# Kernel optimization log

Measured on AMD Instinct MI355X. Metric: run time of the kernel, lower is better.

Reference implementation:

```python
import jax, jax.numpy as jnp
import numpy as np

B, N, K, D_MODEL = 4, 16384, 32, 64

def gather_neighbors(x, idx):
    # x: [B, N, F], idx: [B, N, K] -> [B, N, K, F]
    return jnp.take_along_axis(x[:, :, None, :], idx[:, :, :, None], axis=1)

def setup_inputs() -> dict:
    key = jax.random.key(0)
    k1, k2, k3, k4, k5 = jax.random.split(key, 5)
    x = jax.random.normal(k1, (B, N, D_MODEL), dtype=jnp.float32)
    pos = jax.random.normal(k2, (B, N, 3), dtype=jnp.float32)
    neighbor_idx = jax.random.randint(k3, (B, N, K), 0, N, dtype=jnp.int32)
    W1 = jax.random.normal(k4, (3, D_MODEL), dtype=jnp.float32) * (1.0 / np.sqrt(3.0))
    b1 = jnp.zeros((D_MODEL,), dtype=jnp.float32)
    W2 = jax.random.normal(k5, (D_MODEL, D_MODEL), dtype=jnp.float32) * (1.0 / np.sqrt(D_MODEL))
    b2 = jnp.zeros((D_MODEL,), dtype=jnp.float32)
    return {"x": x, "pos": pos, "neighbor_idx": neighbor_idx,
            "W1": W1, "b1": b1, "W2": W2, "b2": b2}

def reference(x, pos, neighbor_idx, W1, b1, W2, b2):
    # gather neighbor positions: [B, N, K, 3]
    neighbors = gather_neighbors(pos, neighbor_idx)
    rel_pos = pos[:, :, None, :] - neighbors              # [B, N, K, 3]
    # weight MLP: Linear(3,d) + LeakyReLU(0.1), Linear(d,d)
    h = jax.nn.leaky_relu(jnp.einsum('bnkd,df->bnkf', rel_pos, W1) + b1, 0.1)
    w = jnp.einsum('bnkf,fg->bnkg', h, W2) + b2           # [B, N, K, F]
    xg = gather_neighbors(x, neighbor_idx)                # [B, N, K, F]
    return jnp.sum(w * xg, axis=2)                        # [B, N, F]
```

## Files before the change

### kernel.cpp

```cpp
#include <hip/hip_runtime.h>


#define NPTS   16384
#define KNB    32
#define F      64
#define BATCH  4
#define LOG2N  14
#define WPTS   8

typedef _Float16 h2     __attribute__((ext_vector_type(2)));
typedef _Float16 h8     __attribute__((ext_vector_type(8)));
typedef float    f32x16 __attribute__((ext_vector_type(16)));

__global__ __launch_bounds__(256, 2) void pointconv_mfma(
    const float* __restrict__ x,
    const float* __restrict__ pos,
    const int*   __restrict__ idx,
    const float* __restrict__ W1,
    const float* __restrict__ b1,
    const float* __restrict__ W2,
    const float* __restrict__ b2,
    float*       __restrict__ out)
{
    __shared__ __align__(16) _Float16 w1p[32][8];
    __shared__ __align__(16) _Float16 w2f[2][4][2][32][8];

    const int tid = threadIdx.x;
    if (tid < 32) {
        const int g = 2 * tid;
        w1p[tid][0] = (_Float16)W1[0 * F + g]; w1p[tid][1] = (_Float16)W1[0 * F + g + 1];
        w1p[tid][2] = (_Float16)W1[1 * F + g]; w1p[tid][3] = (_Float16)W1[1 * F + g + 1];
        w1p[tid][4] = (_Float16)W1[2 * F + g]; w1p[tid][5] = (_Float16)W1[2 * F + g + 1];
        w1p[tid][6] = (_Float16)b1[g];         w1p[tid][7] = (_Float16)b1[g + 1];
    }
#pragma unroll
    for (int r = 0; r < 16; ++r) {
        const int e = r * 256 + tid;
        const int g = e >> 6, f = e & 63;
        w2f[(g >> 3) & 1][g >> 4][f & 1][f >> 1][g & 7] = (_Float16)W2[e];
    }
    __syncthreads();

    const int lane = tid & 63;
    const int wv   = tid >> 6;
    const int m    = lane & 31;
    const int hf   = lane >> 5;

    const float2 b2v = *(const float2*)(b2 + 2 * m);

    const int p0   = (blockIdx.x * 4 + wv) * WPTS;
    const int p0_s = __builtin_amdgcn_readfirstlane(p0);
    const int base = (p0_s >> LOG2N) << LOG2N;
    const float* __restrict__ xb2 = x + (size_t)base * F + 2 * m;

    int jlo[16], jhi[16];

    {
        const int* __restrict__ rowp = idx + (size_t)p0_s * KNB;
#pragma unroll
        for (int reg = 0; reg < 16; ++reg) {
            const int rA = (reg & 3) + ((reg >> 2) << 3);
            jlo[reg] = rowp[rA];
            jhi[reg] = rowp[rA + 4];
        }
    }
    float2 xvA[16], xvB[16];
#pragma unroll
    for (int reg = 0; reg < 16; ++reg) {
        const int jk = hf ? jhi[reg] : jlo[reg];
        xvA[reg] = *(const float2*)(xb2 + (size_t)jk * F);
    }

    float rx, ry, rz;
    {
        const int jm = idx[p0_s * KNB + m];
        const int nr = base + jm;
        rx = pos[p0_s * 3 + 0] - pos[nr * 3 + 0];
        ry = pos[p0_s * 3 + 1] - pos[nr * 3 + 1];
        rz = pos[p0_s * 3 + 2] - pos[nr * 3 + 2];
    }

    const h2 c01 = { (_Float16)0.1f, (_Float16)0.1f };

#define POINT_BODY(XV_CUR, XV_NXT, I)                                         \
    {                                                                         \
        const int p_s = p0_s + (I);                                           \
        const bool has_next = (I) + 1 < WPTS;                                 \
          \
        if (has_next) {                                                       \
            const int* __restrict__ rowp = idx + (size_t)(p_s + 1) * KNB;     \
            _Pragma("unroll")                                                 \
            for (int reg = 0; reg < 16; ++reg) {                              \
                const int rA = (reg & 3) + ((reg >> 2) << 3);                 \
                jlo[reg] = rowp[rA];                                          \
                jhi[reg] = rowp[rA + 4];                                      \
            }                                                                 \
        }                                                                     \
                                       \
        float rxn = 0.f, ryn = 0.f, rzn = 0.f;                                \
        if (has_next) {                                                       \
            const int jmn = idx[(p_s + 1) * KNB + m];                         \
            const int nr  = base + jmn;                                       \
            rxn = pos[(p_s + 1) * 3 + 0] - pos[nr * 3 + 0];                   \
            ryn = pos[(p_s + 1) * 3 + 1] - pos[nr * 3 + 1];                   \
            rzn = pos[(p_s + 1) * 3 + 2] - pos[nr * 3 + 2];                   \
        }                                                                     \
                      \
        f32x16 acc0, acc1;                                                    \
        _Pragma("unroll")                                                     \
        for (int r = 0; r < 16; ++r) { acc0[r] = b2v.x; acc1[r] = b2v.y; }    \
        const h2 rxp = { (_Float16)rx, (_Float16)rx };                        \
        const h2 ryp = { (_Float16)ry, (_Float16)ry };                        \
        const h2 rzp = { (_Float16)rz, (_Float16)rz };                        \
        _Pragma("unroll")                                                     \
        for (int t = 0; t < 4; ++t) {                                         \
            h8 af;                                                            \
            _Pragma("unroll")                                                 \
            for (int jj = 0; jj < 4; ++jj) {                                  \
                const int g2 = 8 * t + 4 * hf + jj;                           \
                const h8 w = *(const h8*)&w1p[g2][0];                         \
                const h2 wx = __builtin_shufflevector(w, w, 0, 1);            \
                const h2 wy = __builtin_shufflevector(w, w, 2, 3);            \
                const h2 wz = __builtin_shufflevector(w, w, 4, 5);            \
                const h2 bb = __builtin_shufflevector(w, w, 6, 7);            \
                h2 hv = bb + rxp * wx;                                        \
                hv = hv + ryp * wy;                                           \
                hv = hv + rzp * wz;                                           \
                hv = __builtin_elementwise_max(hv, hv * c01);                 \
                af[2 * jj]     = hv[0];                                       \
                af[2 * jj + 1] = hv[1];                                       \
            }                                                                 \
            const h8 bf0 = *(const h8*)&w2f[hf][t][0][m][0];                  \
            const h8 bf1 = *(const h8*)&w2f[hf][t][1][m][0];                  \
            acc0 = __builtin_amdgcn_mfma_f32_32x32x16_f16(af, bf0, acc0, 0, 0, 0); \
            acc1 = __builtin_amdgcn_mfma_f32_32x32x16_f16(af, bf1, acc1, 0, 0, 0); \
        }                                                                     \
              \
        if (has_next) {                                                       \
            _Pragma("unroll")                                                 \
            for (int reg = 0; reg < 16; ++reg) {                              \
                const int jk = hf ? jhi[reg] : jlo[reg];                      \
                XV_NXT[reg] = *(const float2*)(xb2 + (size_t)jk * F);         \
            }                                                                 \
        }                                                                     \
                 \
        float s0 = 0.f, s1 = 0.f;                                             \
        _Pragma("unroll")                                                     \
        for (int reg = 0; reg < 16; ++reg) {                                  \
            s0 = fmaf(acc0[reg], XV_CUR[reg].x, s0);                          \
            s1 = fmaf(acc1[reg], XV_CUR[reg].y, s1);                          \
        }                                                                     \
        s0 += __shfl_xor(s0, 32);                                             \
        s1 += __shfl_xor(s1, 32);                                             \
        if (hf == 0)                                                          \
            *(float2*)(out + (size_t)p_s * F + 2 * m) = make_float2(s0, s1);  \
        rx = rxn; ry = ryn; rz = rzn;                                         \
    }

#pragma unroll 1
    for (int io = 0; io < WPTS; io += 2) {
        POINT_BODY(xvA, xvB, io);
        POINT_BODY(xvB, xvA, io + 1);
    }
#undef POINT_BODY
}

extern "C" void kernel_launch(void* const* d_in, const int* in_sizes, int n_in,
                              void* d_out, int out_size, void* d_ws, size_t ws_size,
                              hipStream_t stream) {
    const float* x   = (const float*)d_in[0];
    const float* pos = (const float*)d_in[1];
    const int*   idx = (const int*)  d_in[2];
    const float* W1  = (const float*)d_in[3];
    const float* b1  = (const float*)d_in[4];
    const float* W2  = (const float*)d_in[5];
    const float* b2  = (const float*)d_in[6];
    float* out = (float*)d_out;

    dim3 grid((BATCH * NPTS) / (4 * WPTS));
    dim3 block(256);
    pointconv_mfma<<<grid, block, 0, stream>>>(x, pos, idx, W1, b1, W2, b2, out);
}
```

Measured before the change: 138.3 us.

## Broadcast neighbor indices via ds_bpermute and deepen index/pos prefetch pipeline

Measured after the change: 409.0 us. +195.6%, slower.

```diff
diff --git a/kernel.cpp b/kernel.cpp
--- a/kernel.cpp
+++ b/kernel.cpp
@@ -12,7 +12,7 @@
 typedef _Float16 h8     __attribute__((ext_vector_type(8)));
 typedef float    f32x16 __attribute__((ext_vector_type(16)));
 
-__global__ __launch_bounds__(256, 2) void pointconv_mfma(
+__global__ __launch_bounds__(256, 3) void pointconv_mfma(
     const float* __restrict__ x,
     const float* __restrict__ pos,
     const int*   __restrict__ idx,
@@ -45,6 +45,7 @@
     const int wv   = tid >> 6;
     const int m    = lane & 31;
     const int hf   = lane >> 5;
+    const int voff = hf << 4;
 
     const float2 b2v = *(const float2*)(b2 + 2 * m);
 
@@ -53,59 +54,53 @@
     const int base = (p0_s >> LOG2N) << LOG2N;
     const float* __restrict__ xb2 = x + (size_t)base * F + 2 * m;
 
-    int jlo[16], jhi[16];
+    const h2 c01 = { (_Float16)0.1f, (_Float16)0.1f };
 
+    float2 xvA[16], xvB[16];
+    float  rlA[6], rlB[6];
+    int    jmA = 0, jmB = 0;
     {
-        const int* __restrict__ rowp = idx + (size_t)p0_s * KNB;
+        const int jm0 = idx[p0_s * KNB + m];
 #pragma unroll
         for (int reg = 0; reg < 16; ++reg) {
             const int rA = (reg & 3) + ((reg >> 2) << 3);
-            jlo[reg] = rowp[rA];
-            jhi[reg] = rowp[rA + 4];
+            const int jk = __builtin_amdgcn_ds_bpermute(voff + 4 * rA, jm0);
+            xvA[reg] = *(const float2*)(xb2 + (size_t)jk * F);
         }
-    }
-    float2 xvA[16], xvB[16];
-#pragma unroll
-    for (int reg = 0; reg < 16; ++reg) {
-        const int jk = hf ? jhi[reg] : jlo[reg];
-        xvA[reg] = *(const float2*)(xb2 + (size_t)jk * F);
+        const int nr0 = base + jm0;
+        rlA[0] = pos[nr0 * 3 + 0]; rlA[1] = pos[nr0 * 3 + 1]; rlA[2] = pos[nr0 * 3 + 2];
+        rlA[3] = pos[p0_s * 3 + 0]; rlA[4] = pos[p0_s * 3 + 1]; rlA[5] = pos[p0_s * 3 + 2];
+        if (WPTS > 1) jmA = idx[(p0_s + 1) * KNB + m];
     }
 
-    float rx, ry, rz;
-    {
-        const int jm = idx[p0_s * KNB + m];
-        const int nr = base + jm;
-        rx = pos[p0_s * 3 + 0] - pos[nr * 3 + 0];
-        ry = pos[p0_s * 3 + 1] - pos[nr * 3 + 1];
-        rz = pos[p0_s * 3 + 2] - pos[nr * 3 + 2];
-    }
-
-    const h2 c01 = { (_Float16)0.1f, (_Float16)0.1f };
-
-#define POINT_BODY(XV_CUR, XV_NXT, I)                                         \
+#define POINT_BODY(XV_CUR, XV_NXT, JM_CUR, JM_NXT, RL_CUR, RL_NXT, I)         \
     {                                                                         \
         const int p_s = p0_s + (I);                                           \
-        const bool has_next = (I) + 1 < WPTS;                                 \
-          \
-        if (has_next) {                                                       \
-            const int* __restrict__ rowp = idx + (size_t)(p_s + 1) * KNB;     \
+                                      \
+        if ((I) + 2 < WPTS) JM_NXT = idx[(p_s + 2) * KNB + m];                \
+           \
+        if ((I) + 1 < WPTS) {                                                 \
+            const int nr = base + JM_CUR;                                     \
+            RL_NXT[0] = pos[nr * 3 + 0];                                      \
+            RL_NXT[1] = pos[nr * 3 + 1];                                      \
+            RL_NXT[2] = pos[nr * 3 + 2];                                      \
+            RL_NXT[3] = pos[(p_s + 1) * 3 + 0];                               \
+            RL_NXT[4] = pos[(p_s + 1) * 3 + 1];                               \
+            RL_NXT[5] = pos[(p_s + 1) * 3 + 2];                               \
+        }                                                                     \
+                    \
+        if ((I) + 1 < WPTS) {                                                 \
             _Pragma("unroll")                                                 \
             for (int reg = 0; reg < 16; ++reg) {                              \
                 const int rA = (reg & 3) + ((reg >> 2) << 3);                 \
-                jlo[reg] = rowp[rA];                                          \
-                jhi[reg] = rowp[rA + 4];                                      \
+                const int jk = __builtin_amdgcn_ds_bpermute(voff + 4 * rA, JM_CUR); \
+                XV_NXT[reg] = *(const float2*)(xb2 + (size_t)jk * F);         \
             }                                                                 \
         }                                                                     \
-                                       \
-        float rxn = 0.f, ryn = 0.f, rzn = 0.f;                                \
-        if (has_next) {                                                       \
-            const int jmn = idx[(p_s + 1) * KNB + m];                         \
-            const int nr  = base + jmn;                                       \
-            rxn = pos[(p_s + 1) * 3 + 0] - pos[nr * 3 + 0];                   \
-            ryn = pos[(p_s + 1) * 3 + 1] - pos[nr * 3 + 1];                   \
-            rzn = pos[(p_s + 1) * 3 + 2] - pos[nr * 3 + 2];                   \
-        }                                                                     \
-                      \
+                \
+        const float rx = RL_CUR[3] - RL_CUR[0];                               \
+        const float ry = RL_CUR[4] - RL_CUR[1];                               \
+        const float rz = RL_CUR[5] - RL_CUR[2];                               \
         f32x16 acc0, acc1;                                                    \
         _Pragma("unroll")                                                     \
         for (int r = 0; r < 16; ++r) { acc0[r] = b2v.x; acc1[r] = b2v.y; }    \
@@ -135,14 +130,6 @@
             acc0 = __builtin_amdgcn_mfma_f32_32x32x16_f16(af, bf0, acc0, 0, 0, 0); \
             acc1 = __builtin_amdgcn_mfma_f32_32x32x16_f16(af, bf1, acc1, 0, 0, 0); \
         }                                                                     \
-              \
-        if (has_next) {                                                       \
-            _Pragma("unroll")                                                 \
-            for (int reg = 0; reg < 16; ++reg) {                              \
-                const int jk = hf ? jhi[reg] : jlo[reg];                      \
-                XV_NXT[reg] = *(const float2*)(xb2 + (size_t)jk * F);         \
-            }                                                                 \
-        }                                                                     \
                  \
         float s0 = 0.f, s1 = 0.f;                                             \
         _Pragma("unroll")                                                     \
@@ -154,13 +141,12 @@
         s1 += __shfl_xor(s1, 32);                                             \
         if (hf == 0)                                                          \
             *(float2*)(out + (size_t)p_s * F + 2 * m) = make_float2(s0, s1);  \
-        rx = rxn; ry = ryn; rz = rzn;                                         \
     }
 
 #pragma unroll 1
     for (int io = 0; io < WPTS; io += 2) {
-        POINT_BODY(xvA, xvB, io);
-        POINT_BODY(xvB, xvA, io + 1);
+        POINT_BODY(xvA, xvB, jmA, jmB, rlA, rlB, io);
+        POINT_BODY(xvB, xvA, jmB, jmA, rlB, rlA, io + 1);
     }
 #undef POINT_BODY
 }
```
